# Optimization experiments

Hardware: AMD Instinct MI355X
Metric: run time of the kernel (lower is better)

Reference implementation:

```python
import jax, jax.numpy as jnp
import numpy as np

B, T, D = 4, 4096, 1024
E, C, O = 8, 1024, 512  # experts, capacity per expert, per-expert out features


def setup_inputs() -> dict:
    key = jax.random.key(0)
    k1, k2, k3, k4 = jax.random.split(key, 4)
    x = jax.random.normal(k1, (B, T, D), dtype=jnp.float32)
    expert_indices = jax.random.randint(k2, (B, E, C), 0, T)
    # nn.Linear(in, out) weight is (out, in) = (E*O, D); reshape -> (E, O, D)
    bound = 1.0 / np.sqrt(D)
    weight = jax.random.uniform(k3, (E, O, D), dtype=jnp.float32, minval=-bound, maxval=bound)
    bias = jax.random.uniform(k4, (E, O), dtype=jnp.float32, minval=-bound, maxval=bound)
    return {"x": x, "expert_indices": expert_indices, "weight": weight, "bias": bias}


def reference(x, expert_indices, weight, bias):
    # gather_experts: select C tokens per (batch, expert) -> (B, E, C, D)
    b_idx = jnp.arange(x.shape[0])[:, None, None]
    selected = x[b_idx, expert_indices]  # (B, E, C, D)
    # per-expert grouped GEMM + bias
    out = jnp.einsum('becd,eod->beco', selected, weight)
    out = out + bias[None, :, None, :]
    return out
```

## Files before the change

### kernel.cpp

```cpp
#include <hip/hip_runtime.h>
#include <stdint.h>

#define Bdim 4
#define Tdim 4096
#define Ddim 1024
#define Edim 8
#define Cdim 1024
#define Odim 512
#define KT 16

using bf16x8 = __attribute__((ext_vector_type(8))) __bf16;
using f32x4  = __attribute__((ext_vector_type(4))) float;

__device__ __forceinline__ unsigned short f2bf(float f) {
  unsigned int u = __float_as_uint(f);
  u += 0x7fffu + ((u >> 16) & 1u);
  return (unsigned short)(u >> 16);
}

__global__ void cast_f32_to_bf16(const float* __restrict__ xin,
                                 const float* __restrict__ win,
                                 unsigned short* __restrict__ outp,
                                 int nx4, int ntot4) {
  int i = blockIdx.x * blockDim.x + threadIdx.x;
  if (i >= ntot4) return;
  float4 v;
  if (i < nx4) v = reinterpret_cast<const float4*>(xin)[i];
  else         v = reinterpret_cast<const float4*>(win)[i - nx4];
  ushort4 o;
  o.x = f2bf(v.x); o.y = f2bf(v.y); o.z = f2bf(v.z); o.w = f2bf(v.w);
  reinterpret_cast<ushort4*>(outp)[i] = o;
}

__device__ __forceinline__ void async_copy16(const unsigned short* g,
                                             unsigned short* l) {
  __builtin_amdgcn_global_load_lds(
      (__attribute__((address_space(1))) unsigned int*)g,
      (__attribute__((address_space(3))) unsigned int*)l, 16, 0, 0);
}

#define FENCE() asm volatile("" ::: "memory")
#define BAR()   do { FENCE(); __builtin_amdgcn_s_barrier(); FENCE(); } while (0)

__global__ __launch_bounds__(512) void moe_mfma_gemm(
    const unsigned short* __restrict__ xbf,
    const unsigned short* __restrict__ wbf,
    const int* __restrict__ idx,
    const float* __restrict__ bias,
    float* __restrict__ out) {
  __shared__ __align__(16) unsigned short sA_e0[128 * 64];
  __shared__ __align__(16) unsigned short sA_e1[128 * 64];
  __shared__ __align__(16) unsigned short sA_o0[128 * 64];
  __shared__ __align__(16) unsigned short sA_o1[128 * 64];
  __shared__ __align__(16) unsigned short sB_e0[128 * 64];
  __shared__ __align__(16) unsigned short sB_e1[128 * 64];
  __shared__ __align__(16) unsigned short sB_o0[128 * 64];
  __shared__ __align__(16) unsigned short sB_o1[128 * 64];

  const int bid = blockIdx.x;
  const int e   = bid & 7;
  const int rr_ = bid >> 3;
  const int nt  = rr_ & 1;
  const int mt  = (rr_ >> 1) & 3;
  const int bb  = rr_ >> 3;
  const int be  = bb * Edim + e;

  const int tid  = threadIdx.x;
  const int lane = tid & 63;
  const int wid  = tid >> 6;
  const int rw   = wid >> 2;
  const int cw   = wid & 3;

  const int rsub = lane >> 3;
  const int kcol = ((lane & 7) ^ rsub) * 8;

  const unsigned short* pA[2][2];
#pragma unroll
  for (int h = 0; h < 2; ++h)
#pragma unroll
    for (int i = 0; i < 2; ++i) {
      const int rr  = h * 128 + wid * 16 + i * 8 + rsub;
      const int tok = idx[be * Cdim + mt * 256 + rr];
      pA[h][i] = xbf + ((size_t)(bb * Tdim + tok)) * Ddim + kcol;
    }
  const unsigned short* pB00 =
      wbf + ((size_t)(e * Odim + nt * 256 + wid * 16 + rsub)) * Ddim + kcol;
  asm volatile("s_waitcnt vmcnt(0)" ::: "memory");

#define STAGE_A_(h, dstArr, koff) do {                                       \
    async_copy16(pA[h][0] + (koff), &dstArr[wid * 16 * 64]);                 \
    async_copy16(pA[h][1] + (koff), &dstArr[(wid * 16 + 8) * 64]);           \
  } while (0)
#define STAGE_B_(h, dstArr, koff) do {                                       \
    async_copy16(pB00 + (h) * 131072 + (koff), &dstArr[wid * 16 * 64]);      \
    async_copy16(pB00 + (h) * 131072 + 8192 + (koff),                        \
                 &dstArr[(wid * 16 + 8) * 64]);                              \
  } while (0)

  STAGE_A_(0, sA_e0, 0);
  STAGE_B_(0, sB_e0, 0);
  STAGE_B_(1, sB_e1, 0);
  STAGE_A_(1, sA_e1, 0);
  STAGE_A_(0, sA_o0, 64);
  STAGE_B_(0, sB_o0, 64);
  STAGE_B_(1, sB_o1, 64);
  asm volatile("s_waitcnt vmcnt(6)" ::: "memory");
  __builtin_amdgcn_s_barrier();
  FENCE();

  const int fr  = lane & 15;
  const int fkc = lane >> 4;
  const int sw  = fr & 7;

  f32x4 acc[2][2][4][2];
#pragma unroll
  for (int a = 0; a < 2; ++a)
#pragma unroll
    for (int bq = 0; bq < 2; ++bq)
#pragma unroll
      for (int im = 0; im < 4; ++im)
#pragma unroll
        for (int in = 0; in < 2; ++in)
          acc[a][bq][im][in] = (f32x4){0.f, 0.f, 0.f, 0.f};

  bf16x8 af[4][2], bf0[2][2], bf1[2][2];

#define LD_A(arr)                                                            \
  _Pragma("unroll")                                                          \
  for (int im = 0; im < 4; ++im)                                             \
    _Pragma("unroll")                                                        \
    for (int kk = 0; kk < 2; ++kk)                                           \
      af[im][kk] = *(const bf16x8*)&arr[(size_t)(rw * 64 + im * 16 + fr) * 64 \
                                        + (((kk * 4 + fkc) ^ sw) * 8)];
#define LD_B(arr, dst)                                                       \
  _Pragma("unroll")                                                          \
  for (int in = 0; in < 2; ++in)                                             \
    _Pragma("unroll")                                                        \
    for (int kk = 0; kk < 2; ++kk)                                           \
      dst[in][kk] = *(const bf16x8*)&arr[(size_t)(cw * 32 + in * 16 + fr) * 64 \
                                         + (((kk * 4 + fkc) ^ sw) * 8)];
#define MFMA16(aq, bq_, B_)                                                  \
  __builtin_amdgcn_s_setprio(1);                                             \
  _Pragma("unroll")                                                          \
  for (int im = 0; im < 4; ++im)                                             \
    _Pragma("unroll")                                                        \
    for (int in = 0; in < 2; ++in)                                           \
      _Pragma("unroll")                                                      \
      for (int kk = 0; kk < 2; ++kk)                                         \
        acc[aq][bq_][im][in] = __builtin_amdgcn_mfma_f32_16x16x32_bf16(      \
            af[im][kk], B_[in][kk], acc[aq][bq_][im][in], 0, 0, 0);          \
  __builtin_amdgcn_s_setprio(0);

  for (int it = 0; it < KT / 2; ++it) {
    const bool g2  = (it < 7);
    const int k1e = (2 * it + 1) * 64;
    const int k2e = (2 * it + 2) * 64;
    const int k1o = (2 * it + 2) * 64;
    const int k2o = (2 * it + 3) * 64;

    LD_A(sA_e0);
    LD_B(sB_e0, bf0);
    STAGE_A_(1, sA_o1, k1e);
    BAR();
    MFMA16(0, 0, bf0);
    BAR();
    LD_B(sB_e1, bf1);
    if (g2) STAGE_A_(0, sA_e0, k2e);
    BAR();
    MFMA16(0, 1, bf1);
    BAR();
    LD_A(sA_e1);
    if (g2) STAGE_B_(0, sB_e0, k2e);
    BAR();
    MFMA16(1, 1, bf1);
    BAR();
    if (g2) STAGE_B_(1, sB_e1, k2e);
    BAR();
    MFMA16(1, 0, bf0);
    if (it == 7) asm volatile("s_waitcnt vmcnt(0)" ::: "memory");
    else         asm volatile("s_waitcnt vmcnt(6)" ::: "memory");
    BAR();

    LD_A(sA_o0);
    LD_B(sB_o0, bf0);
    if (g2) STAGE_A_(1, sA_e1, k1o);
    BAR();
    MFMA16(0, 0, bf0);
    BAR();
    LD_B(sB_o1, bf1);
    if (g2) STAGE_A_(0, sA_o0, k2o);
    BAR();
    MFMA16(0, 1, bf1);
    BAR();
    LD_A(sA_o1);
    if (g2) STAGE_B_(0, sB_o0, k2o);
    BAR();
    MFMA16(1, 1, bf1);
    BAR();
    if (g2) STAGE_B_(1, sB_o1, k2o);
    BAR();
    MFMA16(1, 0, bf0);
    if (g2) asm volatile("s_waitcnt vmcnt(6)" ::: "memory");
    BAR();
  }
#undef STAGE_A_
#undef STAGE_B_
#undef LD_A
#undef LD_B
#undef MFMA16

  const int crow0 = (lane >> 4) * 4;
  float* outBase = out + (size_t)be * (Cdim * Odim)
                 + (size_t)(mt * 256) * Odim + nt * 256;
#pragma unroll
  for (int a = 0; a < 2; ++a)
#pragma unroll
    for (int im = 0; im < 4; ++im) {
      float* prow = outBase + (size_t)(a * 128 + rw * 64 + im * 16 + crow0) * Odim;
#pragma unroll
      for (int bq = 0; bq < 2; ++bq)
#pragma unroll
        for (int in = 0; in < 2; ++in) {
          const int col  = bq * 128 + cw * 32 + in * 16 + fr;
          const float bv = bias[e * Odim + nt * 256 + col];
          float* p = prow + col;
#pragma unroll
          for (int r4 = 0; r4 < 4; ++r4)
            p[(size_t)r4 * Odim] = acc[a][bq][im][in][r4] + bv;
        }
    }
}

extern "C" void kernel_launch(void* const* d_in, const int* in_sizes, int n_in,
                              void* d_out, int out_size, void* d_ws, size_t ws_size,
                              hipStream_t stream) {
  const float* x = (const float*)d_in[0];
  const int* idx = (const int*)d_in[1];
  const float* w = (const float*)d_in[2];
  const float* bias = (const float*)d_in[3];
  float* out = (float*)d_out;

  unsigned short* xbf = (unsigned short*)d_ws;
  unsigned short* wbf = xbf + (size_t)Bdim * Tdim * Ddim;

  const int nx4 = Bdim * Tdim * Ddim / 4;
  const int ntot4 = nx4 + Edim * Odim * Ddim / 4;
  cast_f32_to_bf16<<<(ntot4 + 255) / 256, 256, 0, stream>>>(x, w, xbf, nx4, ntot4);

  moe_mfma_gemm<<<256, 512, 0, stream>>>(xbf, wbf, idx, bias, out);
}
```

Before: 165.9 us.

## Pre-gather tokens into swizzled contiguous bf16 panels before the GEMM

The plain fp32-to-bf16 cast is replaced by a relayout kernel. It gathers the indexed token rows and writes them, along with the weights, into K-tiled panels that already carry the LDS XOR swizzle. The GEMM then streams contiguous 16-byte chunks from these panels and no longer reads indices or does pointer arithmetic. The cost is a larger preprocessing pass: the gathered activation buffer is twice the size of x, so more memory is read and written before the GEMM starts.

```diff
diff --git a/kernel.cpp b/kernel.cpp
--- a/kernel.cpp
+++ b/kernel.cpp
@@ -8,9 +8,11 @@
 #define Cdim 1024
 #define Odim 512
 #define KT 16
+#define PAN 16384
 
 using bf16x8 = __attribute__((ext_vector_type(8))) __bf16;
 using f32x4  = __attribute__((ext_vector_type(4))) float;
+using u16x8  = __attribute__((ext_vector_type(8))) unsigned short;
 
 __device__ __forceinline__ unsigned short f2bf(float f) {
   unsigned int u = __float_as_uint(f);
@@ -18,18 +20,42 @@
   return (unsigned short)(u >> 16);
 }
 
-__global__ void cast_f32_to_bf16(const float* __restrict__ xin,
-                                 const float* __restrict__ win,
-                                 unsigned short* __restrict__ outp,
-                                 int nx4, int ntot4) {
-  int i = blockIdx.x * blockDim.x + threadIdx.x;
-  if (i >= ntot4) return;
-  float4 v;
-  if (i < nx4) v = reinterpret_cast<const float4*>(xin)[i];
-  else         v = reinterpret_cast<const float4*>(win)[i - nx4];
-  ushort4 o;
-  o.x = f2bf(v.x); o.y = f2bf(v.y); o.z = f2bf(v.z); o.w = f2bf(v.w);
-  reinterpret_cast<ushort4*>(outp)[i] = o;
+__global__ void relayout(const float* __restrict__ x,
+                         const float* __restrict__ w,
+                         const int* __restrict__ idx,
+                         unsigned short* __restrict__ Ap,
+                         unsigned short* __restrict__ Wp,
+                         int nA, int nTot) {
+  const int i = blockIdx.x * blockDim.x + threadIdx.x;
+  if (i >= nTot) return;
+  const float* src;
+  unsigned short* dst;
+  if (i < nA) {
+    const int c  = i & 7;
+    const int r  = (i >> 3) & 255;
+    const int kt = (i >> 11) & 15;
+    const int mt = (i >> 15) & 3;
+    const int be = i >> 17;
+    const int bb = be >> 3;
+    const int tok = idx[be * Cdim + mt * 256 + r];
+    src = x + ((size_t)(bb * Tdim + tok)) * Ddim + kt * 64 + ((c ^ (r & 7)) * 8);
+    dst = Ap + (size_t)i * 8;
+  } else {
+    const int j  = i - nA;
+    const int c  = j & 7;
+    const int r  = (j >> 3) & 255;
+    const int kt = (j >> 11) & 15;
+    const int nt = (j >> 15) & 1;
+    const int e  = j >> 16;
+    src = w + ((size_t)(e * Odim + nt * 256 + r)) * Ddim + kt * 64 + ((c ^ (r & 7)) * 8);
+    dst = Wp + (size_t)j * 8;
+  }
+  const float4 v0 = reinterpret_cast<const float4*>(src)[0];
+  const float4 v1 = reinterpret_cast<const float4*>(src)[1];
+  u16x8 o;
+  o[0] = f2bf(v0.x); o[1] = f2bf(v0.y); o[2] = f2bf(v0.z); o[3] = f2bf(v0.w);
+  o[4] = f2bf(v1.x); o[5] = f2bf(v1.y); o[6] = f2bf(v1.z); o[7] = f2bf(v1.w);
+  *reinterpret_cast<u16x8*>(dst) = o;
 }
 
 __device__ __forceinline__ void async_copy16(const unsigned short* g,
@@ -43,9 +69,8 @@
 #define BAR()   do { FENCE(); __builtin_amdgcn_s_barrier(); FENCE(); } while (0)
 
 __global__ __launch_bounds__(512) void moe_mfma_gemm(
-    const unsigned short* __restrict__ xbf,
-    const unsigned short* __restrict__ wbf,
-    const int* __restrict__ idx,
+    const unsigned short* __restrict__ Apan,
+    const unsigned short* __restrict__ Wpan,
     const float* __restrict__ bias,
     float* __restrict__ out) {
   __shared__ __align__(16) unsigned short sA_e0[128 * 64];
@@ -71,29 +96,20 @@
   const int rw   = wid >> 2;
   const int cw   = wid & 3;
 
-  const int rsub = lane >> 3;
-  const int kcol = ((lane & 7) ^ rsub) * 8;
-
-  const unsigned short* pA[2][2];
-#pragma unroll
-  for (int h = 0; h < 2; ++h)
-#pragma unroll
-    for (int i = 0; i < 2; ++i) {
-      const int rr  = h * 128 + wid * 16 + i * 8 + rsub;
-      const int tok = idx[be * Cdim + mt * 256 + rr];
-      pA[h][i] = xbf + ((size_t)(bb * Tdim + tok)) * Ddim + kcol;
-    }
-  const unsigned short* pB00 =
-      wbf + ((size_t)(e * Odim + nt * 256 + wid * 16 + rsub)) * Ddim + kcol;
-  asm volatile("s_waitcnt vmcnt(0)" ::: "memory");
-
-#define STAGE_A_(h, dstArr, koff) do {                                       \
-    async_copy16(pA[h][0] + (koff), &dstArr[wid * 16 * 64]);                 \
-    async_copy16(pA[h][1] + (koff), &dstArr[(wid * 16 + 8) * 64]);           \
+  const unsigned short* Abase = Apan + ((size_t)(be * 4 + mt) * KT) * PAN;
+  const unsigned short* Bbase = Wpan + ((size_t)(e * 2 + nt) * KT) * PAN;
+  const int lo = lane * 8;
+
+#define STAGE_A_(h, dstArr, kt) do {                                         \
+    async_copy16(Abase + (size_t)(kt) * PAN + ((h) * 128 + wid * 16) * 64 + lo, \
+                 &dstArr[wid * 16 * 64]);                                    \
+    async_copy16(Abase + (size_t)(kt) * PAN + ((h) * 128 + wid * 16 + 8) * 64 + lo, \
+                 &dstArr[(wid * 16 + 8) * 64]);                              \
   } while (0)
-#define STAGE_B_(h, dstArr, koff) do {                                       \
-    async_copy16(pB00 + (h) * 131072 + (koff), &dstArr[wid * 16 * 64]);      \
-    async_copy16(pB00 + (h) * 131072 + 8192 + (koff),                        \
+#define STAGE_B_(h, dstArr, kt) do {                                         \
+    async_copy16(Bbase + (size_t)(kt) * PAN + ((h) * 128 + wid * 16) * 64 + lo, \
+                 &dstArr[wid * 16 * 64]);                                    \
+    async_copy16(Bbase + (size_t)(kt) * PAN + ((h) * 128 + wid * 16 + 8) * 64 + lo, \
                  &dstArr[(wid * 16 + 8) * 64]);                              \
   } while (0)
 
@@ -101,9 +117,9 @@
   STAGE_B_(0, sB_e0, 0);
   STAGE_B_(1, sB_e1, 0);
   STAGE_A_(1, sA_e1, 0);
-  STAGE_A_(0, sA_o0, 64);
-  STAGE_B_(0, sB_o0, 64);
-  STAGE_B_(1, sB_o1, 64);
+  STAGE_A_(0, sA_o0, 1);
+  STAGE_B_(0, sB_o0, 1);
+  STAGE_B_(1, sB_o1, 1);
   asm volatile("s_waitcnt vmcnt(6)" ::: "memory");
   __builtin_amdgcn_s_barrier();
   FENCE();
@@ -152,29 +168,28 @@
   __builtin_amdgcn_s_setprio(0);
 
   for (int it = 0; it < KT / 2; ++it) {
-    const bool g2  = (it < 7);
-    const int k1e = (2 * it + 1) * 64;
-    const int k2e = (2 * it + 2) * 64;
-    const int k1o = (2 * it + 2) * 64;
-    const int k2o = (2 * it + 3) * 64;
+    const bool g2 = (it < 7);
+    const int t1e = 2 * it + 1;
+    const int t2e = 2 * it + 2;
+    const int t2o = 2 * it + 3;
 
     LD_A(sA_e0);
     LD_B(sB_e0, bf0);
-    STAGE_A_(1, sA_o1, k1e);
+    STAGE_A_(1, sA_o1, t1e);
     BAR();
     MFMA16(0, 0, bf0);
     BAR();
     LD_B(sB_e1, bf1);
-    if (g2) STAGE_A_(0, sA_e0, k2e);
+    if (g2) STAGE_A_(0, sA_e0, t2e);
     BAR();
     MFMA16(0, 1, bf1);
     BAR();
     LD_A(sA_e1);
-    if (g2) STAGE_B_(0, sB_e0, k2e);
+    if (g2) STAGE_B_(0, sB_e0, t2e);
     BAR();
     MFMA16(1, 1, bf1);
     BAR();
-    if (g2) STAGE_B_(1, sB_e1, k2e);
+    if (g2) STAGE_B_(1, sB_e1, t2e);
     BAR();
     MFMA16(1, 0, bf0);
     if (it == 7) asm volatile("s_waitcnt vmcnt(0)" ::: "memory");
@@ -183,21 +198,21 @@
 
     LD_A(sA_o0);
     LD_B(sB_o0, bf0);
-    if (g2) STAGE_A_(1, sA_e1, k1o);
+    if (g2) STAGE_A_(1, sA_e1, t2e);
     BAR();
     MFMA16(0, 0, bf0);
     BAR();
     LD_B(sB_o1, bf1);
-    if (g2) STAGE_A_(0, sA_o0, k2o);
+    if (g2) STAGE_A_(0, sA_o0, t2o);
     BAR();
     MFMA16(0, 1, bf1);
     BAR();
     LD_A(sA_o1);
-    if (g2) STAGE_B_(0, sB_o0, k2o);
+    if (g2) STAGE_B_(0, sB_o0, t2o);
     BAR();
     MFMA16(1, 1, bf1);
     BAR();
-    if (g2) STAGE_B_(1, sB_o1, k2o);
+    if (g2) STAGE_B_(1, sB_o1, t2o);
     BAR();
     MFMA16(1, 0, bf0);
     if (g2) asm volatile("s_waitcnt vmcnt(6)" ::: "memory");
@@ -240,12 +255,12 @@
   const float* bias = (const float*)d_in[3];
   float* out = (float*)d_out;
 
-  unsigned short* xbf = (unsigned short*)d_ws;
-  unsigned short* wbf = xbf + (size_t)Bdim * Tdim * Ddim;
-
-  const int nx4 = Bdim * Tdim * Ddim / 4;
-  const int ntot4 = nx4 + Edim * Odim * Ddim / 4;
-  cast_f32_to_bf16<<<(ntot4 + 255) / 256, 256, 0, stream>>>(x, w, xbf, nx4, ntot4);
-
-  moe_mfma_gemm<<<256, 512, 0, stream>>>(xbf, wbf, idx, bias, out);
-}
+  unsigned short* Ap = (unsigned short*)d_ws;
+  unsigned short* Wp = Ap + (size_t)Bdim * Edim * Cdim * Ddim;
+
+  const int nA   = Bdim * Edim * Cdim * (Ddim / 8);
+  const int nTot = nA + Edim * Odim * (Ddim / 8);
+  relayout<<<(nTot + 255) / 256, 256, 0, stream>>>(x, w, idx, Ap, Wp, nA, nTot);
+
+  moe_mfma_gemm<<<256, 512, 0, stream>>>(Ap, Wp, bias, out);
+}
```

After: 180.6 us. +8.9%, slower.

## Fuse fp32-to-bf16 conversion into GEMM loads, dropping separate cast kernel

Applied to the files above, without the earlier changes.

Removes the standalone cast kernel that converted all of x and the weights to bf16 in workspace. The GEMM now loads fp32 rows straight from global memory into registers, converts them to bf16 and writes them into swizzled LDS, replacing the async global-to-LDS copies. This saves a full pass over x (including tokens never gathered) and a kernel launch. In exchange it doubles the bytes read per tile, adds conversion VALU work inside the main loop, and raises register pressure from holding the prefetched fp32 values.

```diff
diff --git a/kernel.cpp b/kernel.cpp
--- a/kernel.cpp
+++ b/kernel.cpp
@@ -12,40 +12,13 @@
 using bf16x8 = __attribute__((ext_vector_type(8))) __bf16;
 using f32x4  = __attribute__((ext_vector_type(4))) float;
 
-__device__ __forceinline__ unsigned short f2bf(float f) {
-  unsigned int u = __float_as_uint(f);
-  u += 0x7fffu + ((u >> 16) & 1u);
-  return (unsigned short)(u >> 16);
-}
-
-__global__ void cast_f32_to_bf16(const float* __restrict__ xin,
-                                 const float* __restrict__ win,
-                                 unsigned short* __restrict__ outp,
-                                 int nx4, int ntot4) {
-  int i = blockIdx.x * blockDim.x + threadIdx.x;
-  if (i >= ntot4) return;
-  float4 v;
-  if (i < nx4) v = reinterpret_cast<const float4*>(xin)[i];
-  else         v = reinterpret_cast<const float4*>(win)[i - nx4];
-  ushort4 o;
-  o.x = f2bf(v.x); o.y = f2bf(v.y); o.z = f2bf(v.z); o.w = f2bf(v.w);
-  reinterpret_cast<ushort4*>(outp)[i] = o;
-}
-
-__device__ __forceinline__ void async_copy16(const unsigned short* g,
-                                             unsigned short* l) {
-  __builtin_amdgcn_global_load_lds(
-      (__attribute__((address_space(1))) unsigned int*)g,
-      (__attribute__((address_space(3))) unsigned int*)l, 16, 0, 0);
-}
-
 #define FENCE() asm volatile("" ::: "memory")
 #define BAR()   do { FENCE(); __builtin_amdgcn_s_barrier(); FENCE(); } while (0)
 
 __global__ __launch_bounds__(512) void moe_mfma_gemm(
-    const unsigned short* __restrict__ xbf,
-    const unsigned short* __restrict__ wbf,
+    const float* __restrict__ x,
     const int* __restrict__ idx,
+    const float* __restrict__ w,
     const float* __restrict__ bias,
     float* __restrict__ out) {
   __shared__ __align__(16) unsigned short sA_e0[128 * 64];
@@ -71,42 +44,61 @@
   const int rw   = wid >> 2;
   const int cw   = wid & 3;
 
-  const int rsub = lane >> 3;
-  const int kcol = ((lane & 7) ^ rsub) * 8;
-
-  const unsigned short* pA[2][2];
+  const int rloc = wid * 16 + (lane >> 2);
+  const int csub = (lane & 3) * 16;
+
+  const float4* aP4[2];
+#pragma unroll
+  for (int h = 0; h < 2; ++h) {
+    const int tok = idx[be * Cdim + mt * 256 + h * 128 + rloc];
+    aP4[h] = reinterpret_cast<const float4*>(
+        x + (size_t)(bb * Tdim + tok) * Ddim + csub);
+  }
+  const float4* bP4[2];
 #pragma unroll
   for (int h = 0; h < 2; ++h)
-#pragma unroll
-    for (int i = 0; i < 2; ++i) {
-      const int rr  = h * 128 + wid * 16 + i * 8 + rsub;
-      const int tok = idx[be * Cdim + mt * 256 + rr];
-      pA[h][i] = xbf + ((size_t)(bb * Tdim + tok)) * Ddim + kcol;
-    }
-  const unsigned short* pB00 =
-      wbf + ((size_t)(e * Odim + nt * 256 + wid * 16 + rsub)) * Ddim + kcol;
-  asm volatile("s_waitcnt vmcnt(0)" ::: "memory");
-
-#define STAGE_A_(h, dstArr, koff) do {                                       \
-    async_copy16(pA[h][0] + (koff), &dstArr[wid * 16 * 64]);                 \
-    async_copy16(pA[h][1] + (koff), &dstArr[(wid * 16 + 8) * 64]);           \
+    bP4[h] = reinterpret_cast<const float4*>(
+        w + (size_t)(e * Odim + nt * 256 + h * 128 + rloc) * Ddim + csub);
+
+  const int wr0 = rloc * 64 + (((lane & 3) * 2) ^ (rloc & 7)) * 8;
+  const int wr1 = rloc * 64 + (((lane & 3) * 2 + 1) ^ (rloc & 7)) * 8;
+
+  float4 vA[2][4], vB[2][4];
+
+#define ISSUE_A(t) do {                                                      \
+    _Pragma("unroll")                                                        \
+    for (int h = 0; h < 2; ++h)                                              \
+      _Pragma("unroll")                                                      \
+      for (int i = 0; i < 4; ++i) vA[h][i] = aP4[h][(t) * 16 + i];           \
   } while (0)
-#define STAGE_B_(h, dstArr, koff) do {                                       \
-    async_copy16(pB00 + (h) * 131072 + (koff), &dstArr[wid * 16 * 64]);      \
-    async_copy16(pB00 + (h) * 131072 + 8192 + (koff),                        \
-                 &dstArr[(wid * 16 + 8) * 64]);                              \
+#define ISSUE_B(t) do {                                                      \
+    _Pragma("unroll")                                                        \
+    for (int h = 0; h < 2; ++h)                                              \
+      _Pragma("unroll")                                                      \
+      for (int i = 0; i < 4; ++i) vB[h][i] = bP4[h][(t) * 16 + i];           \
   } while (0)
-
-  STAGE_A_(0, sA_e0, 0);
-  STAGE_B_(0, sB_e0, 0);
-  STAGE_B_(1, sB_e1, 0);
-  STAGE_A_(1, sA_e1, 0);
-  STAGE_A_(0, sA_o0, 64);
-  STAGE_B_(0, sB_o0, 64);
-  STAGE_B_(1, sB_o1, 64);
-  asm volatile("s_waitcnt vmcnt(6)" ::: "memory");
-  __builtin_amdgcn_s_barrier();
-  FENCE();
+#define CVT_WRITE(vreg, arr) do {                                            \
+    bf16x8 lo, hi;                                                           \
+    lo[0] = (__bf16)vreg[0].x; lo[1] = (__bf16)vreg[0].y;                    \
+    lo[2] = (__bf16)vreg[0].z; lo[3] = (__bf16)vreg[0].w;                    \
+    lo[4] = (__bf16)vreg[1].x; lo[5] = (__bf16)vreg[1].y;                    \
+    lo[6] = (__bf16)vreg[1].z; lo[7] = (__bf16)vreg[1].w;                    \
+    hi[0] = (__bf16)vreg[2].x; hi[1] = (__bf16)vreg[2].y;                    \
+    hi[2] = (__bf16)vreg[2].z; hi[3] = (__bf16)vreg[2].w;                    \
+    hi[4] = (__bf16)vreg[3].x; hi[5] = (__bf16)vreg[3].y;                    \
+    hi[6] = (__bf16)vreg[3].z; hi[7] = (__bf16)vreg[3].w;                    \
+    *reinterpret_cast<bf16x8*>(&arr[wr0]) = lo;                              \
+    *reinterpret_cast<bf16x8*>(&arr[wr1]) = hi;                              \
+  } while (0)
+#define WR_A(arr0, arr1) do { CVT_WRITE(vA[0], arr0); CVT_WRITE(vA[1], arr1); } while (0)
+#define WR_B(arr0, arr1) do { CVT_WRITE(vB[0], arr0); CVT_WRITE(vB[1], arr1); } while (0)
+
+  ISSUE_A(0);
+  ISSUE_B(0);
+  WR_A(sA_e0, sA_e1);
+  WR_B(sB_e0, sB_e1);
+  asm volatile("s_waitcnt lgkmcnt(0)" ::: "memory");
+  BAR();
 
   const int fr  = lane & 15;
   const int fkc = lane >> 4;
@@ -152,59 +144,57 @@
   __builtin_amdgcn_s_setprio(0);
 
   for (int it = 0; it < KT / 2; ++it) {
-    const bool g2  = (it < 7);
-    const int k1e = (2 * it + 1) * 64;
-    const int k2e = (2 * it + 2) * 64;
-    const int k1o = (2 * it + 2) * 64;
-    const int k2o = (2 * it + 3) * 64;
+    const bool g = (it < 7);
 
     LD_A(sA_e0);
     LD_B(sB_e0, bf0);
-    STAGE_A_(1, sA_o1, k1e);
+    ISSUE_A(2 * it + 1);
     BAR();
     MFMA16(0, 0, bf0);
     BAR();
     LD_B(sB_e1, bf1);
-    if (g2) STAGE_A_(0, sA_e0, k2e);
+    ISSUE_B(2 * it + 1);
     BAR();
     MFMA16(0, 1, bf1);
     BAR();
     LD_A(sA_e1);
-    if (g2) STAGE_B_(0, sB_e0, k2e);
+    WR_A(sA_o0, sA_o1);
     BAR();
     MFMA16(1, 1, bf1);
     BAR();
-    if (g2) STAGE_B_(1, sB_e1, k2e);
+    WR_B(sB_o0, sB_o1);
     BAR();
     MFMA16(1, 0, bf0);
-    if (it == 7) asm volatile("s_waitcnt vmcnt(0)" ::: "memory");
-    else         asm volatile("s_waitcnt vmcnt(6)" ::: "memory");
+    asm volatile("s_waitcnt lgkmcnt(0)" ::: "memory");
     BAR();
 
     LD_A(sA_o0);
     LD_B(sB_o0, bf0);
-    if (g2) STAGE_A_(1, sA_e1, k1o);
+    if (g) ISSUE_A(2 * it + 2);
     BAR();
     MFMA16(0, 0, bf0);
     BAR();
     LD_B(sB_o1, bf1);
-    if (g2) STAGE_A_(0, sA_o0, k2o);
+    if (g) ISSUE_B(2 * it + 2);
     BAR();
     MFMA16(0, 1, bf1);
     BAR();
     LD_A(sA_o1);
-    if (g2) STAGE_B_(0, sB_o0, k2o);
+    if (g) WR_A(sA_e0, sA_e1);
     BAR();
     MFMA16(1, 1, bf1);
     BAR();
-    if (g2) STAGE_B_(1, sB_o1, k2o);
+    if (g) WR_B(sB_e0, sB_e1);
     BAR();
     MFMA16(1, 0, bf0);
-    if (g2) asm volatile("s_waitcnt vmcnt(6)" ::: "memory");
+    asm volatile("s_waitcnt lgkmcnt(0)" ::: "memory");
     BAR();
   }
-#undef STAGE_A_
-#undef STAGE_B_
+#undef ISSUE_A
+#undef ISSUE_B
+#undef CVT_WRITE
+#undef WR_A
+#undef WR_B
 #undef LD_A
 #undef LD_B
 #undef MFMA16
@@ -239,13 +229,7 @@
   const float* w = (const float*)d_in[2];
   const float* bias = (const float*)d_in[3];
   float* out = (float*)d_out;
-
-  unsigned short* xbf = (unsigned short*)d_ws;
-  unsigned short* wbf = xbf + (size_t)Bdim * Tdim * Ddim;
-
-  const int nx4 = Bdim * Tdim * Ddim / 4;
-  const int ntot4 = nx4 + Edim * Odim * Ddim / 4;
-  cast_f32_to_bf16<<<(ntot4 + 255) / 256, 256, 0, stream>>>(x, w, xbf, nx4, ntot4);
-
-  moe_mfma_gemm<<<256, 512, 0, stream>>>(xbf, wbf, idx, bias, out);
+  (void)d_ws; (void)ws_size;
+
+  moe_mfma_gemm<<<256, 512, 0, stream>>>(x, idx, w, bias, out);
 }
```

New measurement: 297.1 us. 79.0% more time.
